# Performance work log

Hardware: AMD Instinct MI355X
Metric: run time of the kernel (lower is better)

The kernel has to match this reference:

```python
import jax, jax.numpy as jnp
import numpy as np

N_NODES, N_EDGES, D = 50000, 1250000, 64
N_LAYERS = 3


def setup_inputs() -> dict:
    key = jax.random.key(0)
    ks = jax.random.split(key, 6)
    sc = 1.0 / np.sqrt(D)  # ~xavier scale for 64->64 linears
    return {
        "in_feat": jax.random.normal(ks[0], (N_NODES, D), jnp.float32),
        "src": jax.random.randint(ks[1], (N_EDGES,), 0, N_NODES, dtype=jnp.int32),
        "dst": jax.random.randint(ks[2], (N_EDGES,), 0, N_NODES, dtype=jnp.int32),
        "W_pool": jax.random.normal(ks[3], (N_LAYERS, D, D), jnp.float32) * sc,
        "b_pool": jnp.zeros((N_LAYERS, D), jnp.float32),
        "W_self": jax.random.normal(ks[4], (N_LAYERS, D, D), jnp.float32) * sc,
        "W_neigh": jax.random.normal(ks[5], (N_LAYERS, D, D), jnp.float32) * sc,
        "bias": jnp.zeros((N_LAYERS, D), jnp.float32),
    }


def reference(in_feat, src, dst, W_pool, b_pool, W_self, W_neigh, bias):
    # Dropout is identity in eval mode and omitted for determinism.
    n = in_feat.shape[0]
    h = in_feat
    for l in range(N_LAYERS):
        # per-edge pool MLP: relu(W_pool h_src + b_pool)  -> [E, D]
        m = jax.nn.relu(h[src] @ W_pool[l] + b_pool[l])
        # max-pool aggregation over incoming edges of each dst node
        agg = jax.ops.segment_max(m, dst, num_segments=n)
        # nodes with no in-edges get -inf from segment_max -> DGL uses 0
        agg = jnp.where(jnp.isfinite(agg), agg, 0.0)
        h = h @ W_self[l] + agg @ W_neigh[l] + bias[l]
        if l < N_LAYERS - 1:
            h = jax.nn.relu(h)
    return h
```

## Files before the change

### kernel.cpp

```cpp
#include <hip/hip_runtime.h>


#define NN 50000
#define NE 1250000
#define DD 64

#define BSH 8
#define NB1 196
#define CHUNK 8192
#define NBLK1 153

#define GEMM_BLOCKS 782
#define CAST_BLOCKS 400
#define NMAT 9

using bf16x8 = __attribute__((ext_vector_type(8))) short;
using f32x4  = __attribute__((ext_vector_type(4))) float;

__device__ __forceinline__ f32x4 mfma16(bf16x8 a, bf16x8 b, f32x4 c) {
    return __builtin_amdgcn_mfma_f32_16x16x32_bf16(a, b, c, 0, 0, 0);
}

__device__ __forceinline__ unsigned int f32_to_bf16_bits(float f) {
    unsigned int u = __float_as_uint(f);
    return (u + 0x7FFFu + ((u >> 16) & 1u)) >> 16;
}
__device__ __forceinline__ unsigned int pack2bf16(float a, float b) {
    return f32_to_bf16_bits(a) | (f32_to_bf16_bits(b) << 16);
}


__global__ __launch_bounds__(256) void fat1(const int* __restrict__ dst,
                                            int* __restrict__ H,
                                            const float* __restrict__ in_feat,
                                            unsigned short* __restrict__ h0,
                                            const float* __restrict__ Wp,
                                            const float* __restrict__ Ws,
                                            const float* __restrict__ Wn,
                                            unsigned short* __restrict__ wb) {
    __shared__ int hist[NB1];
    int tid = threadIdx.x;
    int bx = blockIdx.x;
    if (bx < NBLK1) {
        for (int i = tid; i < NB1; i += 256) hist[i] = 0;
        __syncthreads();
        int base = bx * CHUNK;
        int end = min(base + CHUNK, NE);
        for (int i = base + tid; i < end; i += 256) atomicAdd(&hist[dst[i] >> BSH], 1);
        __syncthreads();
        for (int k = tid; k < NB1; k += 256) H[k * NBLK1 + bx] = hist[k];
        return;
    }
    if (bx < NBLK1 + CAST_BLOCKS) {
        const float4* inv = (const float4*)in_feat;
        uint4* ov = (uint4*)h0;
        int t = (bx - NBLK1) * 256 + tid;
        for (int u = t; u < (NN * DD) / 8; u += CAST_BLOCKS * 256) {
            float4 f0 = inv[u * 2], f1 = inv[u * 2 + 1];
            uint4 o;
            o.x = pack2bf16(f0.x, f0.y);
            o.y = pack2bf16(f0.z, f0.w);
            o.z = pack2bf16(f1.x, f1.y);
            o.w = pack2bf16(f1.z, f1.w);
            ov[u] = o;
        }
        return;
    }
    int m = bx - NBLK1 - CAST_BLOCKS;
    const float* srcW = (m < 3) ? (Wp + (size_t)m * DD * DD)
                    : (m < 6) ? (Ws + (size_t)(m - 3) * DD * DD)
                              : (Wn + (size_t)(m - 6) * DD * DD);
    unsigned short* dstW = wb + (size_t)m * 512 * 8;
    for (int idx = tid; idx < 512; idx += 256) {
        int lane = idx & 63, cc = (idx >> 6) & 3, s = idx >> 8;
        int col = cc * 16 + (lane & 15);
        int kb = s * 32 + ((lane >> 4) << 3);
#pragma unroll
        for (int j = 0; j < 8; ++j)
            dstW[idx * 8 + j] = (unsigned short)f32_to_bf16_bits(srcW[(kb + j) * DD + col]);
    }
}


__device__ __forceinline__ void load_A(const unsigned short* __restrict__ h,
                                       int row0, int lane, bf16x8& a0, bf16x8& a1) {
    int r = row0 + (lane & 15);
    int kk = (lane >> 4) * 8;
    a0 = bf16x8{0, 0, 0, 0, 0, 0, 0, 0};
    a1 = a0;
    if (r < NN) {
        a0 = *(const bf16x8*)(h + (size_t)r * DD + kk);
        a1 = *(const bf16x8*)(h + (size_t)r * DD + kk + 32);
    }
}


__global__ __launch_bounds__(256) void fat2(const int* __restrict__ H,
                                            int* __restrict__ rowsum,
                                            int* __restrict__ colbase,
                                            int* __restrict__ ticket,
                                            const unsigned short* __restrict__ h0,
                                            const unsigned short* __restrict__ wb,
                                            const float* __restrict__ bp,
                                            unsigned short* __restrict__ z) {
    __shared__ int s[256];
    __shared__ int isLast;
    int tid = threadIdx.x;
    int bx = blockIdx.x;
    if (bx < NB1) {
        int k = bx;
        int v = 0;
        for (int b = tid; b < NBLK1; b += 256) v += H[k * NBLK1 + b];
        s[tid] = v;
        __syncthreads();
        for (int o = 128; o > 0; o >>= 1) {
            if (tid < o) s[tid] += s[tid + o];
            __syncthreads();
        }
        if (tid == 0) {
            atomicExch(&rowsum[k], s[0]);
            __threadfence();
            isLast = (atomicAdd(ticket, 1) == NB1 - 1);
        }
        __syncthreads();
        if (!isLast) return;
        if (tid < 64) {
            int running = 0;
            for (int b0 = 0; b0 < NB1; b0 += 64) {
                int idx = b0 + tid;
                int val = (idx < NB1) ? atomicAdd(&rowsum[idx], 0) : 0;
                int incl = val;
#pragma unroll
                for (int o = 1; o < 64; o <<= 1) {
                    int up = __shfl_up(incl, o);
                    if (tid >= o) incl += up;
                }
                if (idx < NB1) colbase[idx] = running + (incl - val);
                running += __shfl(incl, 63);
            }
            if (tid == 0) colbase[NB1] = running;
        }
        return;
    }
    int lane = tid & 63;
    int row0 = (bx - NB1) * 64 + (tid >> 6) * 16;
    bf16x8 a0, a1;
    load_A(h0, row0, lane, a0, a1);
    const bf16x8* WB = (const bf16x8*)wb;
    f32x4 acc[4];
#pragma unroll
    for (int c = 0; c < 4; ++c) {
        float bv = bp[c * 16 + (lane & 15)];
        acc[c] = f32x4{bv, bv, bv, bv};
        acc[c] = mfma16(a0, WB[(0 * 4 + c) * 64 + lane], acc[c]);
        acc[c] = mfma16(a1, WB[(1 * 4 + c) * 64 + lane], acc[c]);
    }
    int rbase = row0 + (lane >> 4) * 4;
#pragma unroll
    for (int reg = 0; reg < 4; ++reg) {
        int row = rbase + reg;
        if (row < NN) {
#pragma unroll
            for (int c = 0; c < 4; ++c)
                z[(size_t)row * DD + c * 16 + (lane & 15)] =
                    (unsigned short)f32_to_bf16_bits(fmaxf(acc[c][reg], 0.f));
        }
    }
}


__global__ __launch_bounds__(256) void k3_offsets(int* __restrict__ H,
                                                  const int* __restrict__ colbase) {
    int wid = (blockIdx.x * blockDim.x + threadIdx.x) >> 6;
    int lane = threadIdx.x & 63;
    if (wid >= NB1) return;
    int running = colbase[wid];
    int* row = H + wid * NBLK1;
    for (int b0 = 0; b0 < NBLK1; b0 += 64) {
        int idx = b0 + lane;
        int v = (idx < NBLK1) ? row[idx] : 0;
        int incl = v;
#pragma unroll
        for (int o = 1; o < 64; o <<= 1) {
            int up = __shfl_up(incl, o);
            if (lane >= o) incl += up;
        }
        if (idx < NBLK1) row[idx] = running + (incl - v);
        running += __shfl(incl, 63);
    }
}

__global__ __launch_bounds__(256) void p1_scatter(const int* __restrict__ dst,
                                                  const int* __restrict__ src,
                                                  const int* __restrict__ H,
                                                  int* __restrict__ pairs, int e) {
    __shared__ int off[NB1];
    __shared__ int lbase[NB1 + 1];
    __shared__ int cursor[NB1];
    __shared__ int sbuf[2][256];
    __shared__ int sorted[CHUNK];
    int tid = threadIdx.x, bx = blockIdx.x;
    for (int i = tid; i < NB1; i += 256) {
        off[i] = H[i * NBLK1 + bx];
        cursor[i] = 0;
    }
    if (tid < 256) sbuf[0][tid] = 0;
    __syncthreads();
    int base = bx * CHUNK;
    int end = min(base + CHUNK, e);
    int L = end - base;
    for (int i = base + tid; i < end; i += 256) atomicAdd(&sbuf[0][dst[i] >> BSH], 1);
    __syncthreads();
    int myCnt = sbuf[0][tid];
    __syncthreads();
    sbuf[0][tid] = myCnt;
    __syncthreads();
    int cur = 0;
    for (int o = 1; o < 256; o <<= 1) {
        sbuf[cur ^ 1][tid] = sbuf[cur][tid] + ((tid >= o) ? sbuf[cur][tid - o] : 0);
        cur ^= 1;
        __syncthreads();
    }
    if (tid < NB1) lbase[tid] = sbuf[cur][tid] - myCnt;
    if (tid == 0) lbase[NB1] = L;
    __syncthreads();
    for (int i = base + tid; i < end; i += 256) {
        int d = dst[i];
        int k = d >> BSH;
        int r = atomicAdd(&cursor[k], 1);
        sorted[lbase[k] + r] = ((d & 255) << 16) | src[i];
    }
    __syncthreads();
    for (int t = tid; t < L; t += 256) {
        int lo = 0, hi = NB1;
        while (hi - lo > 1) {
            int mid = (lo + hi) >> 1;
            if (t >= lbase[mid]) lo = mid; else hi = mid;
        }
        pairs[off[lo] + (t - lbase[lo])] = sorted[t];
    }
}

__global__ __launch_bounds__(256) void p2_bucket(const int* __restrict__ pairs,
                                                 const int* __restrict__ colbase,
                                                 int* __restrict__ rowptr,
                                                 unsigned short* __restrict__ edge_src) {
    __shared__ int cnt[256];
    __shared__ int base2[256];
    __shared__ int cur2[256];
    __shared__ int sbuf[2][256];
    __shared__ unsigned short stage[16384];
    int k = blockIdx.x;
    int tid = threadIdx.x;
    int beg = colbase[k], end = colbase[k + 1];
    int len = end - beg;
    cnt[tid] = 0;
    cur2[tid] = 0;
    __syncthreads();
    for (int i = beg + tid; i < end; i += 256) atomicAdd(&cnt[pairs[i] >> 16], 1);
    __syncthreads();
    sbuf[0][tid] = cnt[tid];
    __syncthreads();
    int cur = 0;
    for (int o = 1; o < 256; o <<= 1) {
        sbuf[cur ^ 1][tid] = sbuf[cur][tid] + ((tid >= o) ? sbuf[cur][tid - o] : 0);
        cur ^= 1;
        __syncthreads();
    }
    int excl = sbuf[cur][tid] - cnt[tid];
    base2[tid] = excl;
    int node = (k << BSH) + tid;
    if (node < NN) rowptr[node] = beg + excl;
    __syncthreads();
    if (len <= 16384) {
        for (int i = beg + tid; i < end; i += 256) {
            int p = pairs[i];
            int r = atomicAdd(&cur2[p >> 16], 1);
            stage[base2[p >> 16] + r] = (unsigned short)(p & 0xFFFF);
        }
        __syncthreads();
        for (int t = tid; t < len; t += 256) edge_src[beg + t] = stage[t];
    } else {
        for (int i = beg + tid; i < end; i += 256) {
            int p = pairs[i];
            int r = atomicAdd(&cur2[p >> 16], 1);
            edge_src[beg + base2[p >> 16] + r] = (unsigned short)(p & 0xFFFF);
        }
    }
    if (k == 0 && tid == 0) rowptr[NN] = NE;
}


__global__ __launch_bounds__(256) void gemm_fused_mfma(const unsigned short* __restrict__ h,
                                                       const unsigned short* __restrict__ agg,
                                                       const unsigned short* __restrict__ wbs,
                                                       const unsigned short* __restrict__ wbn,
                                                       const unsigned short* __restrict__ wbp,
                                                       const float* __restrict__ b,
                                                       const float* __restrict__ bp,
                                                       unsigned short* __restrict__ hn_out,
                                                       unsigned short* __restrict__ z) {
    __shared__ unsigned short hnl[4][16 * 72];
    int tid = threadIdx.x;
    int w = tid >> 6, lane = tid & 63;
    int row0 = blockIdx.x * 64 + w * 16;
    bf16x8 ah0, ah1, ag0, ag1;
    load_A(h, row0, lane, ah0, ah1);
    load_A(agg, row0, lane, ag0, ag1);
    const bf16x8* WS = (const bf16x8*)wbs;
    const bf16x8* WN = (const bf16x8*)wbn;
    const bf16x8* WP = (const bf16x8*)wbp;
    f32x4 acc[4];
#pragma unroll
    for (int c = 0; c < 4; ++c) {
        float bv = b[c * 16 + (lane & 15)];
        acc[c] = f32x4{bv, bv, bv, bv};
        acc[c] = mfma16(ah0, WS[(0 * 4 + c) * 64 + lane], acc[c]);
        acc[c] = mfma16(ah1, WS[(1 * 4 + c) * 64 + lane], acc[c]);
        acc[c] = mfma16(ag0, WN[(0 * 4 + c) * 64 + lane], acc[c]);
        acc[c] = mfma16(ag1, WN[(1 * 4 + c) * 64 + lane], acc[c]);
    }
    int rloc = (lane >> 4) * 4;
    int rbase = row0 + rloc;
#pragma unroll
    for (int reg = 0; reg < 4; ++reg) {
        int row = rbase + reg;
#pragma unroll
        for (int c = 0; c < 4; ++c) {
            unsigned short us =
                (unsigned short)f32_to_bf16_bits(fmaxf(acc[c][reg], 0.f));
            hnl[w][(rloc + reg) * 72 + c * 16 + (lane & 15)] = us;
            if (row < NN) hn_out[(size_t)row * DD + c * 16 + (lane & 15)] = us;
        }
    }
    int kk = (lane >> 4) * 8;
    bf16x8 p0 = *(const bf16x8*)&hnl[w][(lane & 15) * 72 + kk];
    bf16x8 p1 = *(const bf16x8*)&hnl[w][(lane & 15) * 72 + kk + 32];
    f32x4 acc2[4];
#pragma unroll
    for (int c = 0; c < 4; ++c) {
        float bv = bp[c * 16 + (lane & 15)];
        acc2[c] = f32x4{bv, bv, bv, bv};
        acc2[c] = mfma16(p0, WP[(0 * 4 + c) * 64 + lane], acc2[c]);
        acc2[c] = mfma16(p1, WP[(1 * 4 + c) * 64 + lane], acc2[c]);
    }
#pragma unroll
    for (int reg = 0; reg < 4; ++reg) {
        int row = rbase + reg;
        if (row < NN) {
#pragma unroll
            for (int c = 0; c < 4; ++c)
                z[(size_t)row * DD + c * 16 + (lane & 15)] =
                    (unsigned short)f32_to_bf16_bits(fmaxf(acc2[c][reg], 0.f));
        }
    }
}

__global__ __launch_bounds__(256) void gemm_final_mfma(const unsigned short* __restrict__ h,
                                                       const unsigned short* __restrict__ agg,
                                                       const unsigned short* __restrict__ wbs,
                                                       const unsigned short* __restrict__ wbn,
                                                       const float* __restrict__ b,
                                                       float* __restrict__ out) {
    int tid = threadIdx.x;
    int lane = tid & 63;
    int row0 = blockIdx.x * 64 + (tid >> 6) * 16;
    bf16x8 ah0, ah1, ag0, ag1;
    load_A(h, row0, lane, ah0, ah1);
    load_A(agg, row0, lane, ag0, ag1);
    const bf16x8* WS = (const bf16x8*)wbs;
    const bf16x8* WN = (const bf16x8*)wbn;
    f32x4 acc[4];
#pragma unroll
    for (int c = 0; c < 4; ++c) {
        float bv = b[c * 16 + (lane & 15)];
        acc[c] = f32x4{bv, bv, bv, bv};
        acc[c] = mfma16(ah0, WS[(0 * 4 + c) * 64 + lane], acc[c]);
        acc[c] = mfma16(ah1, WS[(1 * 4 + c) * 64 + lane], acc[c]);
        acc[c] = mfma16(ag0, WN[(0 * 4 + c) * 64 + lane], acc[c]);
        acc[c] = mfma16(ag1, WN[(1 * 4 + c) * 64 + lane], acc[c]);
    }
    int rbase = row0 + (lane >> 4) * 4;
#pragma unroll
    for (int reg = 0; reg < 4; ++reg) {
        int row = rbase + reg;
        if (row < NN) {
#pragma unroll
            for (int c = 0; c < 4; ++c)
                out[(size_t)row * DD + c * 16 + (lane & 15)] = acc[c][reg];
        }
    }
}


__device__ __forceinline__ unsigned int pkmax(unsigned int a, unsigned int b) {
    unsigned int r;
    asm("v_pk_max_u16 %0, %1, %2" : "=v"(r) : "v"(a), "v"(b));
    return r;
}

__global__ __launch_bounds__(256) void agg_max(const unsigned short* __restrict__ z,
                                               const int* __restrict__ rowptr,
                                               const unsigned short* __restrict__ edge_src,
                                               unsigned short* __restrict__ agg, int n) {
    int wslot = __builtin_amdgcn_readfirstlane((int)((blockIdx.x * blockDim.x + threadIdx.x) >> 6));
    int nslots = (gridDim.x * blockDim.x) >> 6;
    int lane = threadIdx.x & 63;
    int eg = lane >> 3;
    int fo = (lane & 7) * 8;
    for (int node = wslot; node < n; node += nslots) {
        int beg = rowptr[node];
        int end = rowptr[node + 1];
        unsigned int m0 = 0, m1 = 0, m2 = 0, m3 = 0;
        int e = beg;
#pragma unroll 2
        for (; e + 8 <= end; e += 8) {
            int s = edge_src[e + eg];
            uint4 a = *(const uint4*)(z + (size_t)s * DD + fo);
            m0 = pkmax(m0, a.x);
            m1 = pkmax(m1, a.y);
            m2 = pkmax(m2, a.z);
            m3 = pkmax(m3, a.w);
        }
        if (e + eg < end) {
            int s = edge_src[e + eg];
            uint4 a = *(const uint4*)(z + (size_t)s * DD + fo);
            m0 = pkmax(m0, a.x);
            m1 = pkmax(m1, a.y);
            m2 = pkmax(m2, a.z);
            m3 = pkmax(m3, a.w);
        }
#pragma unroll
        for (int o = 8; o < 64; o <<= 1) {
            m0 = pkmax(m0, (unsigned int)__shfl_xor((int)m0, o));
            m1 = pkmax(m1, (unsigned int)__shfl_xor((int)m1, o));
            m2 = pkmax(m2, (unsigned int)__shfl_xor((int)m2, o));
            m3 = pkmax(m3, (unsigned int)__shfl_xor((int)m3, o));
        }
        if (eg == 0) {
            uint4 o;
            o.x = m0; o.y = m1; o.z = m2; o.w = m3;
            *(uint4*)(agg + (size_t)node * DD + fo) = o;
        }
    }
}


extern "C" void kernel_launch(void* const* d_in, const int* in_sizes, int n_in,
                              void* d_out, int out_size, void* d_ws, size_t ws_size,
                              hipStream_t stream) {
    const float* in_feat = (const float*)d_in[0];
    const int* src = (const int*)d_in[1];
    const int* dst = (const int*)d_in[2];
    const float* W_pool = (const float*)d_in[3];
    const float* b_pool = (const float*)d_in[4];
    const float* W_self = (const float*)d_in[5];
    const float* W_neigh = (const float*)d_in[6];
    const float* bias = (const float*)d_in[7];
    float* out = (float*)d_out;

    char* ws = (char*)d_ws;
    size_t off = 0;
    auto alloc = [&](size_t bytes) -> void* {
        void* p = (void*)(ws + off);
        off += (bytes + 255) & ~(size_t)255;
        return p;
    };
    int* rowptr              = (int*)alloc((NN + 1) * sizeof(int));
    int* H                   = (int*)alloc((size_t)NB1 * NBLK1 * sizeof(int));
    int* rowsum              = (int*)alloc(NB1 * sizeof(int));
    int* colbase             = (int*)alloc((NB1 + 1) * sizeof(int));
    int* ticket              = (int*)alloc(sizeof(int));
    unsigned short* edge_src = (unsigned short*)alloc((size_t)NE * sizeof(unsigned short));
    unsigned short* z        = (unsigned short*)alloc((size_t)NN * DD * sizeof(unsigned short));
    unsigned short* agg      = (unsigned short*)alloc((size_t)NN * DD * sizeof(unsigned short));
    unsigned short* h0       = (unsigned short*)alloc((size_t)NN * DD * sizeof(unsigned short));
    unsigned short* h1       = (unsigned short*)alloc((size_t)NN * DD * sizeof(unsigned short));
    unsigned short* h2       = (unsigned short*)alloc((size_t)NN * DD * sizeof(unsigned short));
    unsigned short* wb       = (unsigned short*)alloc((size_t)NMAT * 512 * 8 * sizeof(unsigned short));
    int* pairs               = (int*)alloc((size_t)NE * sizeof(int));
    (void)ws_size; (void)in_sizes; (void)n_in; (void)out_size;

    hipMemsetAsync(ticket, 0, sizeof(int), stream);

    auto WBp = [&](int l) { return wb + (size_t)(0 + l) * 4096; };
    auto WBs = [&](int l) { return wb + (size_t)(3 + l) * 4096; };
    auto WBn = [&](int l) { return wb + (size_t)(6 + l) * 4096; };

    fat1<<<NBLK1 + CAST_BLOCKS + NMAT, 256, 0, stream>>>(
        dst, H, in_feat, h0, W_pool, W_self, W_neigh, wb);
    fat2<<<NB1 + GEMM_BLOCKS, 256, 0, stream>>>(
        H, rowsum, colbase, ticket, h0, wb, b_pool, z);
    k3_offsets<<<(NB1 * 64 + 255) / 256, 256, 0, stream>>>(H, colbase);
    p1_scatter<<<NBLK1, 256, 0, stream>>>(dst, src, H, pairs, NE);
    p2_bucket<<<NB1, 256, 0, stream>>>(pairs, colbase, rowptr, edge_src);

    agg_max<<<2048, 256, 0, stream>>>(z, rowptr, edge_src, agg, NN);
    gemm_fused_mfma<<<GEMM_BLOCKS, 256, 0, stream>>>(
        h0, agg, WBs(0), WBn(0), WBp(1), bias, b_pool + DD, h1, z);
    agg_max<<<2048, 256, 0, stream>>>(z, rowptr, edge_src, agg, NN);
    gemm_fused_mfma<<<GEMM_BLOCKS, 256, 0, stream>>>(
        h1, agg, WBs(1), WBn(1), WBp(2), bias + DD, b_pool + 2 * DD, h2, z);
    agg_max<<<2048, 256, 0, stream>>>(z, rowptr, edge_src, agg, NN);
    gemm_final_mfma<<<GEMM_BLOCKS, 256, 0, stream>>>(
        h2, agg, WBs(2), WBn(2), bias + 2 * DD, out);
}
```

Before: 186.7 us.

## Shrink CSR-build buckets and chunks, scan histogram with wave shuffles

The two-pass CSR build now uses 128-node buckets and 2048-edge chunks instead of 256-node buckets and 8192-edge chunks. That roughly quadruples the number of scatter blocks and doubles the number of bucket blocks, which gives more parallelism and smaller shared-memory footprints for better occupancy. The per-chunk histogram prefix sum, which now covers 391 buckets, is done by a single wave with shuffle scans instead of a 256-wide shared-memory scan. The cost is a larger global histogram to scan and more blocks doing the final scatter.

```diff
diff --git a/kernel.cpp b/kernel.cpp
--- a/kernel.cpp
+++ b/kernel.cpp
@@ -5,10 +5,10 @@
 #define NE 1250000
 #define DD 64
 
-#define BSH 8
-#define NB1 196
-#define CHUNK 8192
-#define NBLK1 153
+#define BSH 7
+#define NB1 391
+#define CHUNK 2048
+#define NBLK1 611
 
 #define GEMM_BLOCKS 782
 #define CAST_BLOCKS 400
@@ -195,40 +195,44 @@
                                                   const int* __restrict__ H,
                                                   int* __restrict__ pairs, int e) {
     __shared__ int off[NB1];
+    __shared__ int hcnt[NB1];
+    __shared__ int cursor[NB1];
     __shared__ int lbase[NB1 + 1];
-    __shared__ int cursor[NB1];
-    __shared__ int sbuf[2][256];
     __shared__ int sorted[CHUNK];
     int tid = threadIdx.x, bx = blockIdx.x;
     for (int i = tid; i < NB1; i += 256) {
         off[i] = H[i * NBLK1 + bx];
+        hcnt[i] = 0;
         cursor[i] = 0;
     }
-    if (tid < 256) sbuf[0][tid] = 0;
     __syncthreads();
     int base = bx * CHUNK;
     int end = min(base + CHUNK, e);
     int L = end - base;
-    for (int i = base + tid; i < end; i += 256) atomicAdd(&sbuf[0][dst[i] >> BSH], 1);
-    __syncthreads();
-    int myCnt = sbuf[0][tid];
-    __syncthreads();
-    sbuf[0][tid] = myCnt;
-    __syncthreads();
-    int cur = 0;
-    for (int o = 1; o < 256; o <<= 1) {
-        sbuf[cur ^ 1][tid] = sbuf[cur][tid] + ((tid >= o) ? sbuf[cur][tid - o] : 0);
-        cur ^= 1;
-        __syncthreads();
-    }
-    if (tid < NB1) lbase[tid] = sbuf[cur][tid] - myCnt;
-    if (tid == 0) lbase[NB1] = L;
+    for (int i = base + tid; i < end; i += 256) atomicAdd(&hcnt[dst[i] >> BSH], 1);
+    __syncthreads();
+    if (tid < 64) {
+        int running = 0;
+        for (int b0 = 0; b0 < NB1; b0 += 64) {
+            int idx = b0 + tid;
+            int val = (idx < NB1) ? hcnt[idx] : 0;
+            int incl = val;
+#pragma unroll
+            for (int o = 1; o < 64; o <<= 1) {
+                int up = __shfl_up(incl, o);
+                if (tid >= o) incl += up;
+            }
+            if (idx < NB1) lbase[idx] = running + (incl - val);
+            running += __shfl(incl, 63);
+        }
+        if (tid == 0) lbase[NB1] = L;
+    }
     __syncthreads();
     for (int i = base + tid; i < end; i += 256) {
         int d = dst[i];
         int k = d >> BSH;
         int r = atomicAdd(&cursor[k], 1);
-        sorted[lbase[k] + r] = ((d & 255) << 16) | src[i];
+        sorted[lbase[k] + r] = ((d & 127) << 16) | src[i];
     }
     __syncthreads();
     for (int t = tid; t < L; t += 256) {
@@ -245,34 +249,35 @@
                                                  const int* __restrict__ colbase,
                                                  int* __restrict__ rowptr,
                                                  unsigned short* __restrict__ edge_src) {
-    __shared__ int cnt[256];
-    __shared__ int base2[256];
-    __shared__ int cur2[256];
-    __shared__ int sbuf[2][256];
-    __shared__ unsigned short stage[16384];
+    __shared__ int cnt[128];
+    __shared__ int base2[128];
+    __shared__ int cur2[128];
+    __shared__ int sbuf[2][128];
+    __shared__ unsigned short stage[8192];
     int k = blockIdx.x;
     int tid = threadIdx.x;
     int beg = colbase[k], end = colbase[k + 1];
     int len = end - beg;
-    cnt[tid] = 0;
-    cur2[tid] = 0;
+    if (tid < 128) { cnt[tid] = 0; cur2[tid] = 0; }
     __syncthreads();
     for (int i = beg + tid; i < end; i += 256) atomicAdd(&cnt[pairs[i] >> 16], 1);
     __syncthreads();
-    sbuf[0][tid] = cnt[tid];
+    if (tid < 128) sbuf[0][tid] = cnt[tid];
     __syncthreads();
     int cur = 0;
-    for (int o = 1; o < 256; o <<= 1) {
-        sbuf[cur ^ 1][tid] = sbuf[cur][tid] + ((tid >= o) ? sbuf[cur][tid - o] : 0);
+    for (int o = 1; o < 128; o <<= 1) {
+        if (tid < 128) sbuf[cur ^ 1][tid] = sbuf[cur][tid] + ((tid >= o) ? sbuf[cur][tid - o] : 0);
         cur ^= 1;
         __syncthreads();
     }
-    int excl = sbuf[cur][tid] - cnt[tid];
-    base2[tid] = excl;
-    int node = (k << BSH) + tid;
-    if (node < NN) rowptr[node] = beg + excl;
-    __syncthreads();
-    if (len <= 16384) {
+    if (tid < 128) {
+        int excl = sbuf[cur][tid] - cnt[tid];
+        base2[tid] = excl;
+        int node = (k << BSH) + tid;
+        if (node < NN) rowptr[node] = beg + excl;
+    }
+    __syncthreads();
+    if (len <= 8192) {
         for (int i = beg + tid; i < end; i += 256) {
             int p = pairs[i];
             int r = atomicAdd(&cur2[p >> 16], 1);
```

Result: faster. 173.8 us (-6.9%).
